# Kernel optimization log

Hardware: AMD Instinct MI355X
Metric: run time of the kernel (lower is better)

## Reference

```python
import jax, jax.numpy as jnp
import numpy as np

DECAY = 0.99
EPS = 1e-05
B, C, H, W = 64, 64, 64, 64   # C == embedding_dim
K = 512                       # num_embedding


def setup_inputs() -> dict:
    key = jax.random.key(0)
    k1, k2 = jax.random.split(key)
    inp = jax.random.normal(k1, (B, C, H, W), dtype=jnp.float32)
    embedding = jax.random.normal(k2, (C, K), dtype=jnp.float32)
    cluster_size = jnp.zeros((K,), dtype=jnp.float32)
    embedding_avg = embedding  # buffer initialized as a clone of embedding
    return {"input": inp, "embedding": embedding,
            "cluster_size": cluster_size, "embedding_avg": embedding_avg}


def reference(input, embedding, cluster_size, embedding_avg):
    # NCHW -> NHWC, flatten to [N, C]
    x = jnp.transpose(input, (0, 2, 3, 1))           # [B,H,W,C]
    flat = x.reshape(-1, embedding.shape[0])          # [N,C]
    # squared L2 distances to all K codes: [N,K]
    dist = (jnp.sum(flat * flat, axis=1, keepdims=True)
            - 2.0 * flat @ embedding
            + jnp.sum(embedding * embedding, axis=0, keepdims=True))
    ind = jnp.argmin(dist, axis=1)                    # [N] int
    # gather codes (uses OLD embedding, as in torch)
    quantize = jnp.take(embedding.T, ind, axis=0).reshape(x.shape)  # [B,H,W,C]
    # EMA updates (training branch). Avoid materializing one-hot:
    counts = jnp.zeros((K,), dtype=flat.dtype).at[ind].add(1.0)      # onehot.sum(0)
    embedding_sum = jax.ops.segment_sum(flat, ind, num_segments=K).T  # [C,K] == flat.T @ onehot
    new_cluster_size = cluster_size * DECAY + (1.0 - DECAY) * counts
    new_embedding_avg = embedding_avg * DECAY + (1.0 - DECAY) * embedding_sum
    n = jnp.sum(new_cluster_size)
    cs = (new_cluster_size + EPS) / (n + K * EPS) * n
    new_embedding = new_embedding_avg / cs[None, :]
    # commitment loss and straight-through estimator
    diff = jnp.mean((jax.lax.stop_gradient(quantize) - x) ** 2)
    quantize_st = x + jax.lax.stop_gradient(quantize - x)
    out = jnp.transpose(quantize_st, (0, 3, 1, 2))    # back to NCHW
    embedding_ind = ind.reshape(x.shape[:-1])         # [B,H,W]
    return out, diff, embedding_ind, new_embedding, new_cluster_size, new_embedding_avg
```

## Files before the change

kernel.cpp:

```cpp
#include <hip/hip_runtime.h>
#include <cstdint>
#include <cstddef>

typedef _Float16 half4v __attribute__((ext_vector_type(4)));
typedef _Float16 half8v __attribute__((ext_vector_type(8)));
typedef float    f32x4  __attribute__((ext_vector_type(4)));

#define N_PTS   262144
#define CDIM    64
#define KCODES  512
#define TAUA    5e-3f
#define FLAG_CAP 65536u

#define OFF_DIFF 16777216u
#define OFF_IND  16777217u
#define OFF_EMB  17039361u
#define OFF_CSZ  17072129u
#define OFF_AVG  17072641u

__global__ __launch_bounds__(512) void k_main(
    const float* __restrict__ in, const float* __restrict__ emb,
    float* __restrict__ out,
    int* __restrict__ ind_buf, float* __restrict__ diff_acc,
    unsigned* __restrict__ nflag, int* __restrict__ flaglist)
{
    __shared__ __align__(16) char bsm[133120];
    __shared__ __align__(16) int ind_sh[1024];
    float* ee2_lds = (float*)(bsm + 131072);
    const int tid = threadIdx.x;

    {
        const int col = tid;
        const int xr  = (col & 7) << 4;
        float s = 0.f;
        #pragma unroll
        for (int c0 = 0; c0 < CDIM; c0 += 4) {
            float v[4];
            #pragma unroll
            for (int i = 0; i < 4; ++i) v[i] = emb[(c0 + i)*KCODES + col];
            half4v h, lo;
            #pragma unroll
            for (int i = 0; i < 4; ++i) {
                s = fmaf(v[i], v[i], s);
                _Float16 hh = (_Float16)v[i];
                h[i]  = hh;
                lo[i] = (_Float16)(v[i] - (float)hh);
            }
            const int wb = col*128 + ((c0*2) ^ xr);
            *(half4v*)(bsm + wb)         = h;
            *(half4v*)(bsm + 65536 + wb) = lo;
        }
        ee2_lds[col] = 0.5f * s;
    }
    __syncthreads();

    const int w  = tid >> 6, l = tid & 63;
    const int g  = l >> 4,  lc = l & 15;

    for (int r = 0; r < 2; ++r) {
        const int pbase = (blockIdx.x << 10) + (r << 9) + (w << 6);
        const int b     = pbase >> 12;
        const float* inb = in + ((size_t)b << 18) + ((pbase & 4095) + lc);

        half8v ah[4][2], al[4][2];
        float xs = 0.f;
        #pragma unroll
        for (int t = 0; t < 4; ++t)
            #pragma unroll
            for (int s = 0; s < 2; ++s)
                #pragma unroll
                for (int j = 0; j < 8; ++j) {
                    const int c = s*32 + g*8 + j;
                    const float x = inb[(size_t)c*4096 + t*16];
                    xs = fmaf(x, x, xs);
                    const float xf = -x;
                    const _Float16 hh = (_Float16)xf;
                    ah[t][s][j] = hh;
                    al[t][s][j] = (_Float16)(xf - (float)hh);
                }

        float d1[4][4], d2[4][4]; int k1[4][4];
        #pragma unroll
        for (int t = 0; t < 4; ++t)
            #pragma unroll
            for (int rr = 0; rr < 4; ++rr) { d1[t][rr] = 3.4e38f; d2[t][rr] = 3.4e38f; k1[t][rr] = 0; }

        for (int ct = 0; ct < 32; ++ct) {
            const int col  = (ct << 4) + lc;
            const float sd = ee2_lds[col];
            const int rb   = col*128 + ((g*16) ^ ((col & 7) << 4));
            half8v bh0 = *(const half8v*)(bsm + rb);
            half8v bh1 = *(const half8v*)(bsm + (rb ^ 64));
            half8v bl0 = *(const half8v*)(bsm + 65536 + rb);
            half8v bl1 = *(const half8v*)(bsm + 65536 + (rb ^ 64));

            #pragma unroll
            for (int t = 0; t < 4; ++t) {
                f32x4 acc0 = {sd, sd, sd, sd};
                f32x4 acc1 = {0.f, 0.f, 0.f, 0.f};
                acc0 = __builtin_amdgcn_mfma_f32_16x16x32_f16(al[t][0], bh0, acc0, 0, 0, 0);
                acc1 = __builtin_amdgcn_mfma_f32_16x16x32_f16(al[t][1], bh1, acc1, 0, 0, 0);
                acc0 = __builtin_amdgcn_mfma_f32_16x16x32_f16(ah[t][0], bl0, acc0, 0, 0, 0);
                acc1 = __builtin_amdgcn_mfma_f32_16x16x32_f16(ah[t][1], bl1, acc1, 0, 0, 0);
                acc0 = __builtin_amdgcn_mfma_f32_16x16x32_f16(ah[t][0], bh0, acc0, 0, 0, 0);
                acc1 = __builtin_amdgcn_mfma_f32_16x16x32_f16(ah[t][1], bh1, acc1, 0, 0, 0);
                #pragma unroll
                for (int rr = 0; rr < 4; ++rr) {
                    const float d = acc0[rr] + acc1[rr];
                    const bool cc = d < d1[t][rr];
                    d2[t][rr] = fminf(d2[t][rr], fmaxf(d, d1[t][rr]));
                    d1[t][rr] = fminf(d1[t][rr], d);
                    k1[t][rr] = cc ? col : k1[t][rr];
                }
            }
        }

        #pragma unroll
        for (int m = 1; m <= 8; m <<= 1) {
            #pragma unroll
            for (int t = 0; t < 4; ++t)
                #pragma unroll
                for (int rr = 0; rr < 4; ++rr) {
                    const float od1 = __shfl_xor(d1[t][rr], m);
                    const int   ok1 = __shfl_xor(k1[t][rr], m);
                    const float od2 = __shfl_xor(d2[t][rr], m);
                    const float nd2 = fminf(fmaxf(d1[t][rr], od1), fminf(d2[t][rr], od2));
                    const bool take = (od1 < d1[t][rr]) || (od1 == d1[t][rr] && ok1 < k1[t][rr]);
                    d1[t][rr] = take ? od1 : d1[t][rr];
                    k1[t][rr] = take ? ok1 : k1[t][rr];
                    d2[t][rr] = nd2;
                }
        }

        float ds = 0.f;
        if (lc == 0) {
            #pragma unroll
            for (int t = 0; t < 4; ++t) {
                const int nb = pbase + t*16 + (g << 2);
                int4 iv = make_int4(k1[t][0], k1[t][1], k1[t][2], k1[t][3]);
                *(int4*)(ind_buf + nb) = iv;
                *(int4*)&ind_sh[(r << 9) + (w << 6) + t*16 + (g << 2)] = iv;
                #pragma unroll
                for (int rr = 0; rr < 4; ++rr) {
                    out[OFF_IND + nb + rr] = (float)k1[t][rr];
                    ds += d1[t][rr];
                    if (d2[t][rr] - d1[t][rr] < TAUA) {
                        unsigned ix = atomicAdd(nflag, 1u);
                        if (ix < FLAG_CAP) flaglist[ix] = nb + rr;
                    }
                }
            }
        }
        #pragma unroll
        for (int m = 1; m < 64; m <<= 1) {
            ds += __shfl_xor(ds, m);
            xs += __shfl_xor(xs, m);
        }
        if (l == 0) atomicAdd(diff_acc, 2.f*ds + xs);
    }

    __syncthreads();
    {
        const int n0  = blockIdx.x << 10;
        const int bq  = n0 >> 12;
        const int hw0 = n0 & 4095;
        float* outb = out + ((size_t)bq << 18) + hw0;
        #pragma unroll 4
        for (int it = 0; it < 32; ++it) {
            const int idx = it*512 + tid;
            const int c   = idx >> 8;
            const int p4  = (idx & 255) << 2;
            const int4 iv = *(const int4*)&ind_sh[p4];
            const float* er = emb + (c << 9);
            float4 o = make_float4(er[iv.x], er[iv.y], er[iv.z], er[iv.w]);
            *(float4*)(outb + ((size_t)c << 12) + p4) = o;
        }
    }
}

__global__ void k_refine(const float* __restrict__ in, const float* __restrict__ emb,
                         const unsigned* __restrict__ nflag, const int* __restrict__ flaglist,
                         int* __restrict__ ind_buf, float* __restrict__ out)
{
    const int gtid = blockIdx.x*blockDim.x + threadIdx.x;
    const int wid  = gtid >> 6;
    const int lane = threadIdx.x & 63;
    const int nw   = (gridDim.x * blockDim.x) >> 6;
    unsigned nf = *nflag; if (nf > FLAG_CAP) nf = FLAG_CAP;
    for (unsigned f = wid; f < nf; f += nw) {
        const int n = flaglist[f];
        const int b = n >> 12, hw = n & 4095;
        const float* xb = in + ((size_t)b << 18) + hw;
        const float* er = emb + lane*8;
        double dd[8] = {0,0,0,0,0,0,0,0};
        for (int c = 0; c < CDIM; ++c) {
            const double xv = (double)xb[(size_t)c << 12];
            #pragma unroll
            for (int j = 0; j < 8; ++j) {
                double t = xv - (double)er[c*KCODES + j];
                dd[j] = fma(t, t, dd[j]);
            }
        }
        double bd = 1e300; int bk = 0;
        #pragma unroll
        for (int j = 0; j < 8; ++j) {
            const int kk = lane*8 + j;
            if (dd[j] < bd) { bd = dd[j]; bk = kk; }
        }
        for (int off = 32; off; off >>= 1) {
            double od = __shfl_xor(bd, off);
            int    ok = __shfl_xor(bk, off);
            if (od < bd || (od == bd && ok < bk)) { bd = od; bk = ok; }
        }
        if (lane == 0) { ind_buf[n] = bk; out[OFF_IND + n] = (float)bk; }
        out[((size_t)b << 18) + ((size_t)lane << 12) + hw] = emb[(lane << 9) + bk];
    }
}

__global__ __launch_bounds__(512) void k_stats(const float* __restrict__ in,
    const int* __restrict__ ind_buf, float* __restrict__ p_sum, float* __restrict__ p_cnt)
{
    __shared__ __align__(16) char xsm[2][CDIM*128];
    __shared__ int   ind_lds[2][32];
    __shared__ float s_cnt[KCODES];

    const int tid = threadIdx.x;
    const int wg  = blockIdx.x;
    const int n0  = wg << 10;
    const int b   = n0 >> 12;
    const float* inb = in + ((size_t)b << 18) + (n0 & 4095);

    for (int i = tid; i < KCODES; i += 512) s_cnt[i] = 0.f;

    const int sc  = tid >> 3;
    const int sp  = (tid & 7) << 2;
    const int sxr = (sc & 7) << 4;
    const int wb_hi = sc*128 + ((sp*2) ^ sxr);

    const int w  = tid >> 6, l = tid & 63;
    const int g  = l >> 4,  lc = l & 15;
    const int k0w = w << 6;

    f32x4 acc[4][4];
    #pragma unroll
    for (int ci = 0; ci < 4; ++ci)
        #pragma unroll
        for (int kt = 0; kt < 4; ++kt) acc[ci][kt] = (f32x4){0.f, 0.f, 0.f, 0.f};

    {
        const float4 xv = *(const float4*)(inb + (size_t)sc*4096 + sp);
        half4v h;
        #pragma unroll
        for (int i = 0; i < 4; ++i) h[i] = (_Float16)(((const float*)&xv)[i]);
        *(half4v*)(&xsm[0][0] + wb_hi) = h;
        if (tid < 8) *(int4*)&ind_lds[0][tid*4] = *(const int4*)(ind_buf + n0 + tid*4);
    }

    for (int t = 0; t < 32; ++t) {
        __syncthreads();
        float4 nxt; int4 niv;
        if (t < 31) {
            nxt = *(const float4*)(inb + (size_t)sc*4096 + (t+1)*32 + sp);
            if (tid < 8) niv = *(const int4*)(ind_buf + n0 + (t+1)*32 + tid*4);
        }
        if (tid < 32) atomicAdd(&s_cnt[ind_lds[t & 1][tid]], 1.f);

        const char* xb = &xsm[t & 1][0];
        half8v ah[4];
        #pragma unroll
        for (int ci = 0; ci < 4; ++ci) {
            const int c  = (ci << 4) + lc;
            const int xr = (c & 7) << 4;
            ah[ci] = *(const half8v*)(xb + c*128 + ((g*16) ^ xr));
        }
        int idv[8];
        *(int4*)&idv[0] = *(const int4*)&ind_lds[t & 1][g*8];
        *(int4*)&idv[4] = *(const int4*)&ind_lds[t & 1][g*8 + 4];
        #pragma unroll
        for (int kt = 0; kt < 4; ++kt) {
            const int tgt = k0w + (kt << 4) + lc;
            half8v bf;
            #pragma unroll
            for (int j = 0; j < 8; ++j) bf[j] = (idv[j] == tgt) ? (_Float16)1.0f : (_Float16)0.0f;
            #pragma unroll
            for (int ci = 0; ci < 4; ++ci)
                acc[ci][kt] = __builtin_amdgcn_mfma_f32_16x16x32_f16(ah[ci], bf, acc[ci][kt], 0, 0, 0);
        }
        if (t < 31) {
            half4v h;
            #pragma unroll
            for (int i = 0; i < 4; ++i) h[i] = (_Float16)(((const float*)&nxt)[i]);
            *(half4v*)(&xsm[(t+1) & 1][0] + wb_hi) = h;
            if (tid < 8) *(int4*)&ind_lds[(t+1) & 1][tid*4] = niv;
        }
    }
    __syncthreads();

    float* ps = p_sum + (size_t)wg * (CDIM*KCODES);
    #pragma unroll
    for (int ci = 0; ci < 4; ++ci)
        #pragma unroll
        for (int kt = 0; kt < 4; ++kt)
            #pragma unroll
            for (int rr = 0; rr < 4; ++rr)
                ps[((ci << 4) + (g << 2) + rr)*KCODES + k0w + (kt << 4) + lc] = acc[ci][kt][rr];
    float* pc = p_cnt + wg * KCODES;
    for (int i = tid; i < KCODES; i += 512) pc[i] = s_cnt[i];
}

__global__ __launch_bounds__(256) void k_reduce1(const float* __restrict__ p_sum,
    const float* __restrict__ p_cnt, float* __restrict__ partial8,
    float* __restrict__ cnt8, int wsl)
{
    const int ic = blockIdx.x & 31, ws = blockIdx.x >> 5;
    const int i4 = ic*1024 + threadIdx.x*4;
    const float* base = p_sum + (size_t)ws*wsl*(CDIM*KCODES) + i4;
    float4 s = make_float4(0.f, 0.f, 0.f, 0.f);
    for (int w = 0; w < wsl; ++w) {
        const float4 v = *(const float4*)(base + (size_t)w*(CDIM*KCODES));
        s.x += v.x; s.y += v.y; s.z += v.z; s.w += v.w;
    }
    *(float4*)(partial8 + ws*(CDIM*KCODES) + i4) = s;
    if (ic == 0) {
        for (int k = threadIdx.x; k < KCODES; k += 256) {
            float c = 0.f;
            for (int w = 0; w < wsl; ++w) c += p_cnt[(ws*wsl + w)*KCODES + k];
            cnt8[ws*KCODES + k] = c;
        }
    }
}

__global__ __launch_bounds__(256) void k_reduce2(const float* __restrict__ partial8,
    const float* __restrict__ cnt8, float* __restrict__ sum_tot, float* __restrict__ cnt_tot)
{
    const int i4 = (blockIdx.x*256 + threadIdx.x)*4;
    float4 s = make_float4(0.f, 0.f, 0.f, 0.f);
    #pragma unroll
    for (int p = 0; p < 8; ++p) {
        const float4 v = *(const float4*)(partial8 + p*(CDIM*KCODES) + i4);
        s.x += v.x; s.y += v.y; s.z += v.z; s.w += v.w;
    }
    *(float4*)(sum_tot + i4) = s;
    if (blockIdx.x == 0) {
        for (int k = threadIdx.x; k < KCODES; k += 256) {
            float c = 0.f;
            #pragma unroll
            for (int p = 0; p < 8; ++p) c += cnt8[p*KCODES + k];
            cnt_tot[k] = c;
        }
    }
}

__global__ __launch_bounds__(512) void k_scalars(const float* __restrict__ csz,
    const float* __restrict__ cnt_tot, const float* __restrict__ diff_acc,
    float* __restrict__ out, float* __restrict__ cs_ws)
{
    __shared__ float red[512];
    const int k = threadIdx.x;
    const float ncs = csz[k]*0.99f + 0.01f*cnt_tot[k];
    out[OFF_CSZ + k] = ncs;
    red[k] = ncs;
    __syncthreads();
    for (int s = 256; s > 0; s >>= 1) { if (k < s) red[k] += red[k+s]; __syncthreads(); }
    const float n = red[0];
    cs_ws[k] = (ncs + 1e-5f) / (n + 0.00512f) * n;
    if (k == 0) out[OFF_DIFF] = diff_acc[0] * (1.f/16777216.f);
}

__global__ void k_emb(const float* __restrict__ eavg, const float* __restrict__ sum_tot,
                      const float* __restrict__ cs_ws, float* __restrict__ out)
{
    const int i = blockIdx.x*blockDim.x + threadIdx.x;
    const float avg = eavg[i]*0.99f + 0.01f*sum_tot[i];
    out[OFF_AVG + i] = avg;
    out[OFF_EMB + i] = avg / cs_ws[i & (KCODES-1)];
}

extern "C" void kernel_launch(void* const* d_in, const int* in_sizes, int n_in,
                              void* d_out, int out_size, void* d_ws, size_t ws_size,
                              hipStream_t stream)
{
    const float* in   = (const float*)d_in[0];
    const float* emb  = (const float*)d_in[1];
    const float* csz  = (const float*)d_in[2];
    const float* eavg = (const float*)d_in[3];
    float* out = (float*)d_out;
    char* ws = (char*)d_ws;

    int*      ind      = (int*)(ws + 2048);
    float*    diff_acc = (float*)(ws + 1050624);
    unsigned* nflag    = (unsigned*)(ws + 1050640);
    int*      flaglist = (int*)(ws + 1050656);
    float*    cs_ws    = (float*)(ws + 1312800);
    float*    cnt_tot  = (float*)(ws + 1314848);
    float*    sum_tot  = (float*)(ws + 1316896);
    const size_t off_part = 1447968;
    const int swgs = 256;
    float* p_sum    = (float*)(ws + off_part);
    float* p_cnt    = (float*)(ws + off_part + (size_t)swgs*(CDIM*KCODES)*4);
    float* partial8 = (float*)(ws + off_part + (size_t)swgs*133120);
    float* cnt8     = (float*)(ws + off_part + (size_t)swgs*133120 + 1048576);

    hipMemsetAsync(ws + 1050624, 0, 32, stream);

    hipLaunchKernelGGL(k_main,    dim3(256),   dim3(512), 0, stream, in, emb, out, ind, diff_acc, nflag, flaglist);
    hipLaunchKernelGGL(k_refine,  dim3(256),   dim3(256), 0, stream, in, emb, nflag, flaglist, ind, out);
    hipLaunchKernelGGL(k_stats,   dim3(256),   dim3(512), 0, stream, in, ind, p_sum, p_cnt);
    hipLaunchKernelGGL(k_reduce1, dim3(256),   dim3(256), 0, stream, p_sum, p_cnt, partial8, cnt8, swgs >> 3);
    hipLaunchKernelGGL(k_reduce2, dim3(32),    dim3(256), 0, stream, partial8, cnt8, sum_tot, cnt_tot);
    hipLaunchKernelGGL(k_scalars, dim3(1),     dim3(512), 0, stream, csz, cnt_tot, diff_acc, out, cs_ws);
    hipLaunchKernelGGL(k_emb,     dim3(128),   dim3(256), 0, stream, eavg, sum_tot, cs_ws, out);
}
```

Before: 221.5 us.

## Move quantize gather to separate kernel and fuse final reduction kernels

```diff
diff --git a/kernel.cpp b/kernel.cpp
--- a/kernel.cpp
+++ b/kernel.cpp
@@ -25,7 +25,6 @@
     unsigned* __restrict__ nflag, int* __restrict__ flaglist)
 {
     __shared__ __align__(16) char bsm[133120];
-    __shared__ __align__(16) int ind_sh[1024];
     float* ee2_lds = (float*)(bsm + 131072);
     const int tid = threadIdx.x;
 
@@ -139,7 +138,6 @@
                 const int nb = pbase + t*16 + (g << 2);
                 int4 iv = make_int4(k1[t][0], k1[t][1], k1[t][2], k1[t][3]);
                 *(int4*)(ind_buf + nb) = iv;
-                *(int4*)&ind_sh[(r << 9) + (w << 6) + t*16 + (g << 2)] = iv;
                 #pragma unroll
                 for (int rr = 0; rr < 4; ++rr) {
                     out[OFF_IND + nb + rr] = (float)k1[t][rr];
@@ -157,24 +155,6 @@
             xs += __shfl_xor(xs, m);
         }
         if (l == 0) atomicAdd(diff_acc, 2.f*ds + xs);
-    }
-
-    __syncthreads();
-    {
-        const int n0  = blockIdx.x << 10;
-        const int bq  = n0 >> 12;
-        const int hw0 = n0 & 4095;
-        float* outb = out + ((size_t)bq << 18) + hw0;
-        #pragma unroll 4
-        for (int it = 0; it < 32; ++it) {
-            const int idx = it*512 + tid;
-            const int c   = idx >> 8;
-            const int p4  = (idx & 255) << 2;
-            const int4 iv = *(const int4*)&ind_sh[p4];
-            const float* er = emb + (c << 9);
-            float4 o = make_float4(er[iv.x], er[iv.y], er[iv.z], er[iv.w]);
-            *(float4*)(outb + ((size_t)c << 12) + p4) = o;
-        }
     }
 }
 
@@ -213,7 +193,6 @@
             if (od < bd || (od == bd && ok < bk)) { bd = od; bk = ok; }
         }
         if (lane == 0) { ind_buf[n] = bk; out[OFF_IND + n] = (float)bk; }
-        out[((size_t)b << 18) + ((size_t)lane << 12) + hw] = emb[(lane << 9) + bk];
     }
 }
 
@@ -330,50 +309,62 @@
     }
 }
 
-__global__ __launch_bounds__(256) void k_reduce2(const float* __restrict__ partial8,
-    const float* __restrict__ cnt8, float* __restrict__ sum_tot, float* __restrict__ cnt_tot)
-{
-    const int i4 = (blockIdx.x*256 + threadIdx.x)*4;
-    float4 s = make_float4(0.f, 0.f, 0.f, 0.f);
+__global__ __launch_bounds__(512) void k_final(const float* __restrict__ partial8,
+    const float* __restrict__ cnt8, const float* __restrict__ csz,
+    const float* __restrict__ eavg, const float* __restrict__ diff_acc,
+    float* __restrict__ out)
+{
+    __shared__ float red[512];
+    __shared__ float cs_lds[512];
+    const int k = threadIdx.x;
+    float c = 0.f;
     #pragma unroll
-    for (int p = 0; p < 8; ++p) {
-        const float4 v = *(const float4*)(partial8 + p*(CDIM*KCODES) + i4);
-        s.x += v.x; s.y += v.y; s.z += v.z; s.w += v.w;
-    }
-    *(float4*)(sum_tot + i4) = s;
-    if (blockIdx.x == 0) {
-        for (int k = threadIdx.x; k < KCODES; k += 256) {
-            float c = 0.f;
-            #pragma unroll
-            for (int p = 0; p < 8; ++p) c += cnt8[p*KCODES + k];
-            cnt_tot[k] = c;
-        }
-    }
-}
-
-__global__ __launch_bounds__(512) void k_scalars(const float* __restrict__ csz,
-    const float* __restrict__ cnt_tot, const float* __restrict__ diff_acc,
-    float* __restrict__ out, float* __restrict__ cs_ws)
-{
-    __shared__ float red[512];
-    const int k = threadIdx.x;
-    const float ncs = csz[k]*0.99f + 0.01f*cnt_tot[k];
-    out[OFF_CSZ + k] = ncs;
+    for (int p = 0; p < 8; ++p) c += cnt8[p*KCODES + k];
+    const float ncs = csz[k]*0.99f + 0.01f*c;
+    if (blockIdx.x == 0) out[OFF_CSZ + k] = ncs;
     red[k] = ncs;
     __syncthreads();
     for (int s = 256; s > 0; s >>= 1) { if (k < s) red[k] += red[k+s]; __syncthreads(); }
     const float n = red[0];
-    cs_ws[k] = (ncs + 1e-5f) / (n + 0.00512f) * n;
-    if (k == 0) out[OFF_DIFF] = diff_acc[0] * (1.f/16777216.f);
-}
-
-__global__ void k_emb(const float* __restrict__ eavg, const float* __restrict__ sum_tot,
-                      const float* __restrict__ cs_ws, float* __restrict__ out)
-{
-    const int i = blockIdx.x*blockDim.x + threadIdx.x;
-    const float avg = eavg[i]*0.99f + 0.01f*sum_tot[i];
-    out[OFF_AVG + i] = avg;
-    out[OFF_EMB + i] = avg / cs_ws[i & (KCODES-1)];
+    cs_lds[k] = (ncs + 1e-5f) / (n + 0.00512f) * n;
+    if (blockIdx.x == 0 && k == 0) out[OFF_DIFF] = diff_acc[0] * (1.f/16777216.f);
+    __syncthreads();
+    if (k < 256) {
+        const int i = (blockIdx.x*256 + k)*4;
+        float4 s4 = make_float4(0.f, 0.f, 0.f, 0.f);
+        #pragma unroll
+        for (int p = 0; p < 8; ++p) {
+            const float4 v = *(const float4*)(partial8 + p*(CDIM*KCODES) + i);
+            s4.x += v.x; s4.y += v.y; s4.z += v.z; s4.w += v.w;
+        }
+        const float4 ea = *(const float4*)(eavg + i);
+        const float a0 = ea.x*0.99f + 0.01f*s4.x;
+        const float a1 = ea.y*0.99f + 0.01f*s4.y;
+        const float a2 = ea.z*0.99f + 0.01f*s4.z;
+        const float a3 = ea.w*0.99f + 0.01f*s4.w;
+        const int kb = i & (KCODES-1);
+        out[OFF_AVG + i]     = a0;  out[OFF_AVG + i + 1] = a1;
+        out[OFF_AVG + i + 2] = a2;  out[OFF_AVG + i + 3] = a3;
+        out[OFF_EMB + i]     = a0 / cs_lds[kb];
+        out[OFF_EMB + i + 1] = a1 / cs_lds[kb + 1];
+        out[OFF_EMB + i + 2] = a2 / cs_lds[kb + 2];
+        out[OFF_EMB + i + 3] = a3 / cs_lds[kb + 3];
+    }
+}
+
+__global__ void k_quant(const float* __restrict__ emb, const int* __restrict__ ind_buf,
+                        float* __restrict__ out)
+{
+    const int gid = blockIdx.x*blockDim.x + threadIdx.x;
+    const int i  = gid << 2;
+    const int hw = i & 4095;
+    const int c  = (i >> 12) & 63;
+    const int b  = i >> 18;
+    const int n  = (b << 12) + hw;
+    const int4 iv = *(const int4*)(ind_buf + n);
+    const float* er = emb + (c << 9);
+    float4 o = make_float4(er[iv.x], er[iv.y], er[iv.z], er[iv.w]);
+    *(float4*)(out + i) = o;
 }
 
 extern "C" void kernel_launch(void* const* d_in, const int* in_sizes, int n_in,
@@ -391,9 +382,6 @@
     float*    diff_acc = (float*)(ws + 1050624);
     unsigned* nflag    = (unsigned*)(ws + 1050640);
     int*      flaglist = (int*)(ws + 1050656);
-    float*    cs_ws    = (float*)(ws + 1312800);
-    float*    cnt_tot  = (float*)(ws + 1314848);
-    float*    sum_tot  = (float*)(ws + 1316896);
     const size_t off_part = 1447968;
     const int swgs = 256;
     float* p_sum    = (float*)(ws + off_part);
@@ -405,9 +393,8 @@
 
     hipLaunchKernelGGL(k_main,    dim3(256),   dim3(512), 0, stream, in, emb, out, ind, diff_acc, nflag, flaglist);
     hipLaunchKernelGGL(k_refine,  dim3(256),   dim3(256), 0, stream, in, emb, nflag, flaglist, ind, out);
+    hipLaunchKernelGGL(k_quant,   dim3(16384), dim3(256), 0, stream, emb, ind, out);
     hipLaunchKernelGGL(k_stats,   dim3(256),   dim3(512), 0, stream, in, ind, p_sum, p_cnt);
     hipLaunchKernelGGL(k_reduce1, dim3(256),   dim3(256), 0, stream, p_sum, p_cnt, partial8, cnt8, swgs >> 3);
-    hipLaunchKernelGGL(k_reduce2, dim3(32),    dim3(256), 0, stream, partial8, cnt8, sum_tot, cnt_tot);
-    hipLaunchKernelGGL(k_scalars, dim3(1),     dim3(512), 0, stream, csz, cnt_tot, diff_acc, out, cs_ws);
-    hipLaunchKernelGGL(k_emb,     dim3(128),   dim3(256), 0, stream, eavg, sum_tot, cs_ws, out);
-}
+    hipLaunchKernelGGL(k_final,   dim3(32),    dim3(512), 0, stream, partial8, cnt8, csz, eavg, diff_acc, out);
+}
```

After: 209.5 us. 1.06x faster.
